# Performance work log

Hardware: AMD Instinct MI355X
Metric: run time of the kernel (lower is better)

The kernel has to match this reference:

```python
import jax, jax.numpy as jnp
import numpy as np

WS = 8          # window_size
NH = 8          # num_heads
IQKV = 128      # inner_qk_v_dim
IQKC = 32       # inner_qk_c_dim
IVV = 64        # inner_v_v_dim
EPS = 1e-6
B, HH, WW, DV, DC = 2, 224, 224, 256, 64


def _rmsnorm(x, g):
    return x * jax.lax.rsqrt(jnp.mean(x * x, axis=-1, keepdims=True) + EPS) * g


def _window(x):
    # (b, h, w, d) -> (b, Wh, Ww, ws*ws, d)
    b, h, w, d = x.shape
    x = x.reshape(b, h // WS, WS, w // WS, WS, d).transpose(0, 1, 3, 2, 4, 5)
    return x.reshape(b, h // WS, w // WS, WS * WS, d)


def _unwindow(x, h, w):
    # (b, N, ws*ws, d) -> (b, h, w, d)
    b, _, _, d = x.shape
    x = x.reshape(b, h // WS, w // WS, WS, WS, d).transpose(0, 1, 3, 2, 4, 5)
    return x.reshape(b, h, w, d)


def _source_qkv(V, C, Wqk_v, bqk_v, g_v, Wqk_c, bqk_c, g_c, Wv):
    Vw, Cw = _window(V), _window(C)          # (b, Wh, Ww, n, d)
    b, Wh, Ww, n, _ = Vw.shape
    N = Wh * Ww
    Vavg, Cavg = Vw.mean(-2), Cw.mean(-2)
    qk_v = _rmsnorm(Vavg @ Wqk_v + bqk_v, g_v)   # (b, Wh, Ww, 2*IQKV)
    qk_c = _rmsnorm(Cavg @ Wqk_c + bqk_c, g_c)   # (b, Wh, Ww, 2*IQKC)
    # 'b Wh Ww (H e) -> b H (Wh Ww) e' then chunk2 along e
    qk_v = qk_v.reshape(b, N, NH, -1).transpose(0, 2, 1, 3)
    qk_c = qk_c.reshape(b, N, NH, -1).transpose(0, 2, 1, 3)
    ev, ec = qk_v.shape[-1] // 2, qk_c.shape[-1] // 2
    qv, kv = qk_v[..., :ev], qk_v[..., ev:]
    qc, kc = qk_c[..., :ec], qk_c[..., ec:]
    # value projection: 'b Wh Ww n (e H) -> b H (Wh Ww) (n e)'
    e = IVV // NH
    Vv = (Vw @ Wv).reshape(b, N, n, e, NH).transpose(0, 4, 1, 2, 3).reshape(b, NH, N, n * e)
    return qv, kv, qc, kc, Vv, (Wh, Ww)


def _forward(values0, coords0, values1, coords1,
             Wqk_v, bqk_v, g_v, Wqk_c, bqk_c, g_c, Wv, Wback):
    parts = [_source_qkv(V, C, Wqk_v, bqk_v, g_v, Wqk_c, bqk_c, g_c, Wv)
             for V, C in ((values0, coords0), (values1, coords1))]
    qv = jnp.concatenate([p[0] for p in parts], axis=2)
    kv = jnp.concatenate([p[1] for p in parts], axis=2)
    qc = jnp.concatenate([p[2] for p in parts], axis=2)
    kc = jnp.concatenate([p[3] for p in parts], axis=2)
    Vv = jnp.concatenate([p[4] for p in parts], axis=2)
    scores = (jnp.einsum('bhqe,bhke->bhqk', qv, kv) / jnp.sqrt(jnp.float32(IQKV))
              + jnp.einsum('bhqe,bhke->bhqk', qc, kc) / jnp.sqrt(jnp.float32(IQKC)))
    A = jax.nn.softmax(scores, axis=-1)            # (b, H, N, N)
    rw = jnp.einsum('bhqk,bhkf->bhqf', A, Vv)      # (b, H, N, n*e)
    b, _, N, _ = rw.shape
    n, e = WS * WS, IVV // NH
    # 'b H N (n e) -> b N n (e H)'
    rw = rw.reshape(b, NH, N, n, e).transpose(0, 2, 3, 4, 1).reshape(b, N, n, e * NH)
    rw = rw @ Wback                                # (b, N, n, Dv)
    outs, off = [], 0
    for (V, _), p in zip(((values0, coords0), (values1, coords1)), parts):
        Wh, Ww = p[5]
        Ns = Wh * Ww
        outs.append(_unwindow(rw[:, off:off + Ns], Wh * WS, Ww * WS))
        off += Ns
    return tuple(outs)


def setup_inputs() -> dict:
    key = jax.random.key(0)
    ks = jax.random.split(key, 8)
    s = 0.02
    return {
        'values0': jax.random.normal(ks[0], (B, HH, WW, DV), jnp.float32),
        'coords0': jax.random.normal(ks[1], (B, HH, WW, DC), jnp.float32),
        'values1': jax.random.normal(ks[2], (B, HH, WW, DV), jnp.float32),
        'coords1': jax.random.normal(ks[3], (B, HH, WW, DC), jnp.float32),
        'Wqk_v': s * jax.random.normal(ks[4], (DV, 2 * IQKV), jnp.float32),
        'bqk_v': jnp.zeros((2 * IQKV,), jnp.float32),
        'g_v': jnp.ones((2 * IQKV,), jnp.float32),
        'Wqk_c': s * jax.random.normal(ks[5], (DC, 2 * IQKC), jnp.float32),
        'bqk_c': jnp.zeros((2 * IQKC,), jnp.float32),
        'g_c': jnp.ones((2 * IQKC,), jnp.float32),
        'Wv': s * jax.random.normal(ks[6], (DV, IVV), jnp.float32),
        'Wback': s * jax.random.normal(ks[7], (IVV, DV), jnp.float32),
    }


def reference(values0, coords0, values1, coords1,
              Wqk_v, bqk_v, g_v, Wqk_c, bqk_c, g_c, Wv, Wback):
    return _forward(values0, coords0, values1, coords1,
                    Wqk_v, bqk_v, g_v, Wqk_c, bqk_c, g_c, Wv, Wback)
```

## Files before the change

### kernel.cpp

```cpp
#include <hip/hip_runtime.h>

#define NSRC 784
#define NTOT 1568
#define NHD 8
#define DVC 256
#define DCC 64
#define D20 20
#define FDIM 512
#define OUT_PER_SRC 25690112

typedef short s16x8 __attribute__((ext_vector_type(8)));
typedef unsigned short u16x8 __attribute__((ext_vector_type(8)));
typedef unsigned short u16x4 __attribute__((ext_vector_type(4)));
typedef float f32x4 __attribute__((ext_vector_type(4)));
typedef float f32x16 __attribute__((ext_vector_type(16)));
typedef unsigned u32x4 __attribute__((ext_vector_type(4)));

__device__ __forceinline__ unsigned short f2bf(float x) {
    unsigned u = __float_as_uint(x);
    unsigned r = (u + 0x7FFFu + ((u >> 16) & 1u)) >> 16;
    return (unsigned short)r;
}

__device__ __forceinline__ unsigned cvt_pk_bf16(float lo, float hi) {
    unsigned r;
    asm volatile("v_cvt_pk_bf16_f32 %0, %1, %2" : "=v"(r) : "v"(lo), "v"(hi));
    return r;
}

__device__ __forceinline__ void split_bf(float x, unsigned short& hi, unsigned short& lo) {
    unsigned short h = f2bf(x);
    float hf = __uint_as_float(((unsigned)h) << 16);
    hi = h;
    lo = f2bf(x - hf);
}

__global__ __launch_bounds__(256) void kz_zero(unsigned short* __restrict__ p) {
    size_t i = (size_t)blockIdx.x * 256 + threadIdx.x;
    u16x8 z = (u16x8)0;
    *(u16x8*)&p[i * 8] = z;
}

__global__ __launch_bounds__(256) void k0c_wvpack(
    const float* __restrict__ Wv, unsigned short* __restrict__ Wvp) {
    int idx = blockIdx.x * 256 + threadIdx.x;
    int j = idx & 7, lane = (idx >> 3) & 63, hl = (idx >> 9) & 1;
    int c = (idx >> 10) & 7, mi = idx >> 13;
    int e = mi * 16 + (lane & 15);
    int dd = c * 32 + (lane >> 4) * 8 + j;
    unsigned short h, l;
    split_bf(Wv[dd * DCC + e], h, l);
    Wvp[idx] = hl ? l : h;
}

__global__ __launch_bounds__(256) void k0b_wback(
    const float* __restrict__ Wb, unsigned short* __restrict__ Wp) {
    int idx = blockIdx.x * 256 + threadIdx.x;
    int jj = idx & 7, lane = (idx >> 3) & 63, hl = (idx >> 9) & 1;
    int kc = (idx >> 10) & 1, mt = idx >> 11;
    int c = mt * 16 + (lane & 15);
    int j = kc * 32 + (lane >> 4) * 8 + jj;
    unsigned short h, l;
    split_bf(Wb[j * 256 + c], h, l);
    Wp[idx] = hl ? l : h;
}

__global__ __launch_bounds__(256) void k1c_avg(
    const float* __restrict__ c0, const float* __restrict__ c1,
    float* __restrict__ Cavg) {
    int wi = blockIdx.x * 4 + (threadIdx.x >> 6);
    int d = threadIdx.x & 63;
    int b = wi / NTOT, N = wi % NTOT;
    int src = N / NSRC, nloc = N % NSRC;
    int wh = nloc / 28, ww = nloc % 28;
    const float* __restrict__ C = src ? c1 : c0;
    int pbase = (b * 224 + wh * 8) * 224 + ww * 8;
    float s = 0.f;
#pragma unroll 8
    for (int p = 0; p < 64; ++p)
        s += C[(size_t)(pbase + (p >> 3) * 224 + (p & 7)) * DCC + d];
    Cavg[(size_t)wi * DCC + d] = s * 0.015625f;
}

__global__ __launch_bounds__(256) void k2_qk(
    const float* __restrict__ Vavg, const float* __restrict__ Cavg,
    const float* __restrict__ Wqkv, const float* __restrict__ bqkv, const float* __restrict__ gv,
    const float* __restrict__ Wqkc, const float* __restrict__ bqkc, const float* __restrict__ gc,
    unsigned short* __restrict__ Qp, unsigned short* __restrict__ Kp) {
    __shared__ float xv[DVC];
    __shared__ float xc[DCC];
    __shared__ float wred[4];
    int blk = blockIdx.x;
    int b = blk / NTOT, N = blk % NTOT;
    int t = threadIdx.x;
    int tile = N >> 5, l31 = N & 31;
    xv[t] = Vavg[(size_t)blk * DVC + t];
    if (t < DCC) xc[t] = Cavg[(size_t)blk * DCC + t];
    __syncthreads();
    float yv = bqkv[t];
#pragma unroll 4
    for (int d = 0; d < DVC; ++d) yv += xv[d] * Wqkv[d * 256 + t];
    float ss = yv * yv;
#pragma unroll
    for (int off = 32; off; off >>= 1) ss += __shfl_xor(ss, off, 64);
    if ((t & 63) == 0) wred[t >> 6] = ss;
    __syncthreads();
    float tot = wred[0] + wred[1] + wred[2] + wred[3];
    float rv = rsqrtf(tot * (1.f / 256.f) + 1e-6f);
    float yn = yv * rv * gv[t];
    int h = t >> 5, c = t & 31;
    int bh = b * NHD + h;
    {
        int isq = (c < 16);
        int d = isq ? c : c - 16;
        float val = isq ? yn * 0.088388347648318447f : yn;
        unsigned short h16, l16;
        split_bf(val, h16, l16);
        int hh = d >> 3, j = d & 7;
        size_t base = ((size_t)(bh * 49 + tile) * 4) * 512 + (size_t)(hh * 32 + l31) * 8 + j;
        unsigned short* dst = isq ? Qp : Kp;
        dst[base] = h16;
        dst[base + 1024] = l16;
    }
    if (t < DCC) {
        float yc = bqkc[t];
#pragma unroll 4
        for (int d = 0; d < DCC; ++d) yc += xc[d] * Wqkc[d * 64 + t];
        float sc = yc * yc;
#pragma unroll
        for (int off = 32; off; off >>= 1) sc += __shfl_xor(sc, off, 64);
        float rc = rsqrtf(sc * (1.f / 64.f) + 1e-6f);
        float ycn = yc * rc * gc[t];
        int h2 = t >> 3, c2 = t & 7;
        int bh2 = b * NHD + h2;
        int isq = (c2 < 4);
        int dd = isq ? c2 : c2 - 4;
        float val = isq ? ycn * 0.17677669529663687f : ycn;
        unsigned short h16, l16;
        split_bf(val, h16, l16);
        size_t base = ((size_t)(bh2 * 49 + tile) * 4 + 1) * 512 + (size_t)l31 * 8 + dd;
        unsigned short* dst = isq ? Qp : Kp;
        dst[base] = h16;
        dst[base + 1024] = l16;
    }
}

__global__ __launch_bounds__(256) void k3_vv(
    const float* __restrict__ v0, const float* __restrict__ v1,
    const unsigned short* __restrict__ Wvp,
    unsigned short* __restrict__ Vvb, float* __restrict__ Vavg) {
    __shared__ unsigned short eb[64 * 66];
    __shared__ float avgw[1024];
    int blk = blockIdx.x;
    int b = blk / NTOT, N = blk % NTOT;
    int src = N / NSRC, nloc = N % NSRC;
    int wh = nloc / 28, ww = nloc % 28;
    const float* __restrict__ V = src ? v1 : v0;
    int t = threadIdx.x;
    int w = t >> 6, lane = t & 63;
    int lm = lane & 15, lk = lane >> 4;
    int px = w * 16 + lm;
    int pbase = (b * 224 + wh * 8) * 224 + ww * 8;
    const float* __restrict__ xrow =
        V + (size_t)(pbase + (px >> 3) * 224 + (px & 7)) * DVC + lk * 8;

    f32x4 acc[4];
#pragma unroll
    for (int mi = 0; mi < 4; ++mi) acc[mi] = (f32x4)0.f;

#pragma unroll
    for (int c = 0; c < 8; ++c) {
        float4 x0 = *(const float4*)&xrow[c * 32];
        float4 x1 = *(const float4*)&xrow[c * 32 + 4];
        float xv8[8] = {x0.x, x0.y, x0.z, x0.w, x1.x, x1.y, x1.z, x1.w};
        u16x8 bhu, blu;
#pragma unroll
        for (int j = 0; j < 8; ++j) {
            unsigned short hq, lq;
            split_bf(xv8[j], hq, lq);
            bhu[j] = hq; blu[j] = lq;
        }
        s16x8 xhi = __builtin_bit_cast(s16x8, bhu);
        s16x8 xlo = __builtin_bit_cast(s16x8, blu);
        float sv[8] = {xv8[0], xv8[1], xv8[2], xv8[3], xv8[4], xv8[5], xv8[6], xv8[7]};
#pragma unroll
        for (int off = 1; off <= 8; off <<= 1)
#pragma unroll
            for (int j = 0; j < 8; ++j) sv[j] += __shfl_xor(sv[j], off, 64);
        if (lm == 0) {
#pragma unroll
            for (int j = 0; j < 8; ++j)
                avgw[w * 256 + c * 32 + lk * 8 + j] = sv[j];
        }
#pragma unroll
        for (int mi = 0; mi < 4; ++mi) {
            const unsigned short* Wf = Wvp + (size_t)((mi * 8 + c) * 2) * 512 + lane * 8;
            s16x8 Ah = *(const s16x8*)&Wf[0];
            s16x8 Al = *(const s16x8*)&Wf[512];
            acc[mi] = __builtin_amdgcn_mfma_f32_16x16x32_bf16(Ah, xlo, acc[mi], 0, 0, 0);
            acc[mi] = __builtin_amdgcn_mfma_f32_16x16x32_bf16(Al, xhi, acc[mi], 0, 0, 0);
            acc[mi] = __builtin_amdgcn_mfma_f32_16x16x32_bf16(Ah, xhi, acc[mi], 0, 0, 0);
        }
    }
#pragma unroll
    for (int mi = 0; mi < 4; ++mi) {
#pragma unroll
        for (int r = 0; r < 4; ++r) {
            int e = mi * 16 + lk * 4 + r;
            eb[px * 66 + e] = f2bf(acc[mi][r]);
        }
    }
    __syncthreads();
    unsigned short* dst = Vvb + (size_t)blk * 4096;
#pragma unroll
    for (int i = 0; i < 2; ++i) {
        int flat16 = i * 256 + t;
        int f3 = flat16 >> 6;
        int h = (flat16 >> 3) & 7;
        int px8 = (flat16 & 7) * 8;
        u16x8 vv;
#pragma unroll
        for (int u = 0; u < 8; ++u) vv[u] = eb[(px8 + u) * 66 + f3 * 8 + h];
        *(u16x8*)&dst[flat16 * 8] = vv;
    }
    Vavg[(size_t)blk * DVC + t] =
        (avgw[t] + avgw[256 + t] + avgw[512 + t] + avgw[768 + t]) * 0.015625f;
}

__global__ __launch_bounds__(256) void k3b_pack(
    const unsigned short* __restrict__ Vvb, unsigned short* __restrict__ Vp) {
    __shared__ unsigned short tile[32 * 576];
    int kt = blockIdx.x, bh = blockIdx.y;
    int b = bh >> 3, h = bh & 7;
    int t = threadIdx.x;
#pragma unroll
    for (int it = 0; it < 8; ++it) {
        int flat = it * 256 + t;
        int r5 = flat >> 6;
        int c = flat & 63;
        int f3 = c >> 3, px8 = (c & 7) * 8;
        const unsigned short* s =
            Vvb + ((size_t)(b * NTOT + kt * 32 + r5) * 8 + f3) * 512 + h * 64 + px8;
        *(u16x8*)&tile[r5 * 576 + f3 * 72 + px8] = *(const u16x8*)s;
    }
    __syncthreads();
    unsigned short* dst = Vp + ((size_t)bh * 49 + kt) * 16384;
#pragma unroll
    for (int it = 0; it < 8; ++it) {
        int flato = it * 256 + t;
        int lane = flato & 63;
        int kh = (flato >> 6) & 1;
        int sub = (flato >> 7) & 3;
        int w = flato >> 9;
        int l31 = lane & 31, hh = lane >> 5;
        int f = w * 128 + sub * 32 + l31;
        int kbase = kh * 16 + hh * 8;
        u16x8 v;
#pragma unroll
        for (int j = 0; j < 8; ++j)
            v[j] = tile[(kbase + j) * 576 + (f & 7) * 72 + (f >> 3)];
        *(u16x8*)&dst[(size_t)flato * 8] = v;
    }
}

__global__ __launch_bounds__(256) void k4_attn(
    const unsigned short* __restrict__ Qp, const unsigned short* __restrict__ Kp,
    const unsigned short* __restrict__ Vp, float* __restrict__ rw) {
    __shared__ float ebuf[32 * 132];
    int wg = blockIdx.x;
    int qt = wg >> 4, bh = wg & 15;
    int q0 = qt * 32;
    int t = threadIdx.x;
    int w = t >> 6, lane = t & 63;
    int l31 = lane & 31, hh = lane >> 5;

    const unsigned short* __restrict__ Qpb = Qp + ((size_t)(bh * 49 + qt) * 4) * 512 + lane * 8;
    const unsigned short* __restrict__ Kpb = Kp + (size_t)bh * 49 * 2048 + lane * 8;
    const unsigned short* __restrict__ Vpb = Vp + (size_t)bh * 49 * 16384 + lane * 8;

    s16x8 qa0 = *(const s16x8*)&Qpb[0];
    s16x8 qa1 = *(const s16x8*)&Qpb[512];
    s16x8 ql0 = *(const s16x8*)&Qpb[1024];
    s16x8 ql1 = *(const s16x8*)&Qpb[1536];

    s16x8 ka0 = *(const s16x8*)&Kpb[0];
    s16x8 ka1 = *(const s16x8*)&Kpb[512];
    s16x8 kl0 = *(const s16x8*)&Kpb[1024];
    s16x8 kl1 = *(const s16x8*)&Kpb[1536];

    float m = -1e30f, lsum = 0.f;
    f32x16 acc[4];
#pragma unroll
    for (int s = 0; s < 4; ++s) acc[s] = (f32x16)0.f;

    for (int kt = 0; kt < NTOT / 32; ++kt) {
        const unsigned short* Vtile = Vpb + (size_t)kt * 16384 + (w * 8) * 512;
        s16x8 va[8];
#pragma unroll
        for (int fr = 0; fr < 8; ++fr)
            va[fr] = *(const s16x8*)&Vtile[fr * 512];
        int ktn = (kt < 48) ? kt + 1 : 48;
        const unsigned short* Ktn = Kpb + (size_t)ktn * 2048;
        s16x8 kn0 = *(const s16x8*)&Ktn[0];
        s16x8 kn1 = *(const s16x8*)&Ktn[512];
        s16x8 kn2 = *(const s16x8*)&Ktn[1024];
        s16x8 kn3 = *(const s16x8*)&Ktn[1536];

        f32x16 sacc = (f32x16)0.f;
        sacc = __builtin_amdgcn_mfma_f32_32x32x16_bf16(kl0, qa0, sacc, 0, 0, 0);
        sacc = __builtin_amdgcn_mfma_f32_32x32x16_bf16(ka0, ql0, sacc, 0, 0, 0);
        sacc = __builtin_amdgcn_mfma_f32_32x32x16_bf16(ka0, qa0, sacc, 0, 0, 0);
        sacc = __builtin_amdgcn_mfma_f32_32x32x16_bf16(kl1, qa1, sacc, 0, 0, 0);
        sacc = __builtin_amdgcn_mfma_f32_32x32x16_bf16(ka1, ql1, sacc, 0, 0, 0);
        sacc = __builtin_amdgcn_mfma_f32_32x32x16_bf16(ka1, qa1, sacc, 0, 0, 0);

        float tmax = sacc[0];
#pragma unroll
        for (int r = 1; r < 16; ++r) tmax = fmaxf(tmax, sacc[r]);
        tmax = fmaxf(tmax, __shfl_xor(tmax, 32, 64));
        if (__any(tmax > m + 8.f)) {
            float mn = fmaxf(m, tmax);
            float sc = __expf(m - mn);
#pragma unroll
            for (int s = 0; s < 4; ++s) acc[s] = acc[s] * sc;
            lsum *= sc;
            m = mn;
        }
        unsigned P2[8];
        float tsum = 0.f;
#pragma unroll
        for (int j = 0; j < 8; ++j) {
            float pa = __expf(sacc[2 * j] - m);
            float pb = __expf(sacc[2 * j + 1] - m);
            tsum += pa + pb;
            P2[j] = cvt_pk_bf16(pa, pb);
        }
        lsum += tsum + __shfl_xor(tsum, 32, 64);
        unsigned X2[8];
#pragma unroll
        for (int j = 0; j < 8; ++j) X2[j] = (unsigned)__shfl_xor((int)P2[j], 32, 64);
        u32x4 b0u, b1u;
        if (hh == 0) {
            b0u[0] = P2[0]; b0u[1] = P2[1]; b0u[2] = X2[0]; b0u[3] = X2[1];
            b1u[0] = P2[4]; b1u[1] = P2[5]; b1u[2] = X2[4]; b1u[3] = X2[5];
        } else {
            b0u[0] = X2[2]; b0u[1] = X2[3]; b0u[2] = P2[2]; b0u[3] = P2[3];
            b1u[0] = X2[6]; b1u[1] = X2[7]; b1u[2] = P2[6]; b1u[3] = P2[7];
        }
        s16x8 pb0 = __builtin_bit_cast(s16x8, b0u);
        s16x8 pb1 = __builtin_bit_cast(s16x8, b1u);

#pragma unroll
        for (int sub = 0; sub < 4; ++sub) {
            acc[sub] = __builtin_amdgcn_mfma_f32_32x32x16_bf16(va[2 * sub],     pb0, acc[sub], 0, 0, 0);
            acc[sub] = __builtin_amdgcn_mfma_f32_32x32x16_bf16(va[2 * sub + 1], pb1, acc[sub], 0, 0, 0);
        }
        ka0 = kn0; ka1 = kn1; kl0 = kn2; kl1 = kn3;
    }

    float inv = 1.f / lsum;
    float* rwg = rw + ((size_t)bh * NTOT + q0) * FDIM;
#pragma unroll
    for (int c = 0; c < 4; ++c) {
        __syncthreads();
        if (w == c) {
#pragma unroll
            for (int sub = 0; sub < 4; ++sub) {
#pragma unroll
                for (int r = 0; r < 16; ++r) {
                    int fl = sub * 32 + (r & 3) + 8 * (r >> 2) + 4 * hh;
                    ebuf[l31 * 132 + fl] = acc[sub][r] * inv;
                }
            }
        }
        __syncthreads();
        int qr = t >> 3, cb = (t & 7) * 16;
#pragma unroll
        for (int j = 0; j < 4; ++j) {
            *(float4*)&rwg[(size_t)qr * FDIM + c * 128 + cb + j * 4] =
                *(const float4*)&ebuf[qr * 132 + cb + j * 4];
        }
    }
}

__global__ __launch_bounds__(256) void k5_back(
    const float* __restrict__ rw, const unsigned short* __restrict__ Wp,
    float* __restrict__ out) {
    __shared__ unsigned short SB[2 * 64 * 72];
    unsigned short* BhL = SB;
    unsigned short* BlL = SB + 64 * 72;
    int blk = blockIdx.x;
    int b = blk / NTOT, N = blk % NTOT;
    int src = N / NSRC, nloc = N % NSRC;
    int wh = nloc / 28, ww = nloc % 28;
    int t = threadIdx.x;
    int w = t >> 6, lane = t & 63;
    int lm = lane & 15, lk = lane >> 4;
    int pbase = (b * 224 + wh * 8) * 224 + ww * 8;

#pragma unroll
    for (int i = 0; i < 4; ++i) {
        int flat4 = i * 256 + t;
        int h = flat4 >> 7;
        int f0 = (flat4 & 127) * 4;
        float4 v = *(const float4*)&rw[((size_t)(b * NHD + h) * NTOT + N) * FDIM + f0];
        int n = f0 >> 3;
        int ebase = f0 & 7;
        float vv[4] = {v.x, v.y, v.z, v.w};
#pragma unroll
        for (int u = 0; u < 4; ++u) {
            int j8 = ebase + u;
            unsigned short h16, l16;
            split_bf(vv[u], h16, l16);
            int col = ((j8 ^ (n & 7)) << 3) | h;
            BhL[n * 72 + col] = h16;
            BlL[n * 72 + col] = l16;
        }
    }
    __syncthreads();

    f32x4 acc[4][4];
#pragma unroll
    for (int mi = 0; mi < 4; ++mi)
#pragma unroll
        for (int nt = 0; nt < 4; ++nt) acc[mi][nt] = (f32x4)0.f;

    const unsigned short* Wpw = Wp + (size_t)(w * 4) * 2048 + lane * 8;
#pragma unroll
    for (int kc = 0; kc < 2; ++kc) {
        s16x8 Ah[4], Al[4], Bh4[4], Bl4[4];
#pragma unroll
        for (int mi = 0; mi < 4; ++mi) {
            int base = mi * 2048 + kc * 1024;
            Ah[mi] = *(const s16x8*)&Wpw[base];
            Al[mi] = *(const s16x8*)&Wpw[base + 512];
        }
#pragma unroll
        for (int nt = 0; nt < 4; ++nt) {
            int n = nt * 16 + lm;
            int addr = n * 72 + (((kc * 4 + lk) ^ (n & 7)) << 3);
            Bh4[nt] = *(const s16x8*)&BhL[addr];
            Bl4[nt] = *(const s16x8*)&BlL[addr];
        }
#pragma unroll
        for (int mi = 0; mi < 4; ++mi)
#pragma unroll
            for (int nt = 0; nt < 4; ++nt) {
                acc[mi][nt] = __builtin_amdgcn_mfma_f32_16x16x32_bf16(Ah[mi], Bl4[nt], acc[mi][nt], 0, 0, 0);
                acc[mi][nt] = __builtin_amdgcn_mfma_f32_16x16x32_bf16(Al[mi], Bh4[nt], acc[mi][nt], 0, 0, 0);
                acc[mi][nt] = __builtin_amdgcn_mfma_f32_16x16x32_bf16(Ah[mi], Bh4[nt], acc[mi][nt], 0, 0, 0);
            }
    }

    float* eb = (float*)SB;
    float* outp = out + (size_t)src * OUT_PER_SRC;
#pragma unroll
    for (int ch = 0; ch < 4; ++ch) {
        __syncthreads();
        if (w == ch) {
#pragma unroll
            for (int mi = 0; mi < 4; ++mi)
#pragma unroll
                for (int nt = 0; nt < 4; ++nt)
#pragma unroll
                    for (int r = 0; r < 4; ++r) {
                        int n = nt * 16 + lm;
                        int cl = mi * 16 + lk * 4 + r;
                        eb[n * 68 + cl] = acc[mi][nt][r];
                    }
        }
        __syncthreads();
#pragma unroll
        for (int i = 0; i < 4; ++i) {
            int fl4 = i * 256 + t;
            int n = fl4 >> 4, c4 = (fl4 & 15) * 4;
            int opix = pbase + (n >> 3) * 224 + (n & 7);
            *(float4*)&outp[(size_t)opix * DVC + ch * 64 + c4] =
                *(const float4*)&eb[n * 68 + c4];
        }
    }
}

extern "C" void kernel_launch(void* const* d_in, const int* in_sizes, int n_in,
                              void* d_out, int out_size, void* d_ws, size_t ws_size,
                              hipStream_t stream) {
    const float* v0   = (const float*)d_in[0];
    const float* c0   = (const float*)d_in[1];
    const float* v1   = (const float*)d_in[2];
    const float* c1   = (const float*)d_in[3];
    const float* Wqkv = (const float*)d_in[4];
    const float* bqkv = (const float*)d_in[5];
    const float* gv   = (const float*)d_in[6];
    const float* Wqkc = (const float*)d_in[7];
    const float* bqkc = (const float*)d_in[8];
    const float* gc   = (const float*)d_in[9];
    const float* Wv   = (const float*)d_in[10];
    const float* Wbk  = (const float*)d_in[11];

    float* ws = (float*)d_ws;
    float* rw   = ws;
    float* Vavg = ws;
    float* Cavg = ws + 802816;
    unsigned short* Qp   = (unsigned short*)(ws + 12845056);
    unsigned short* Kp   = (unsigned short*)(ws + 13647872);
    unsigned short* Wvp  = (unsigned short*)(ws + 14450688);
    unsigned short* Vvb  = (unsigned short*)(ws + 14467072);
    unsigned short* Vp   = (unsigned short*)(ws + 20889600);
    unsigned short* Wp   = (unsigned short*)(ws + 27312128);

    float* outp = (float*)d_out;

    kz_zero   <<<1568, 256, 0, stream>>>(Qp);
    k0c_wvpack<<<256, 256, 0, stream>>>(Wv, Wvp);
    k0b_wback <<<256, 256, 0, stream>>>(Wbk, Wp);
    k3_vv     <<<2 * NTOT, 256, 0, stream>>>(v0, v1, Wvp, Vvb, Vavg);
    k1c_avg   <<<784, 256, 0, stream>>>(c0, c1, Cavg);
    k2_qk     <<<2 * NTOT, 256, 0, stream>>>(Vavg, Cavg, Wqkv, bqkv, gv, Wqkc, bqkc, gc, Qp, Kp);
    k3b_pack  <<<dim3(49, 16), 256, 0, stream>>>(Vvb, Vp);
    k4_attn   <<<784, 256, 0, stream>>>(Qp, Kp, Vp, rw);
    k5_back   <<<2 * NTOT, 256, 0, stream>>>(rw, Wp, outp);
}
```

Baseline: 335.6 us.

## Use exp2 softmax with folded log2e, permlane32 swap, drop K prefetch

Folds log2(e) into the query scaling so the attention softmax can use exp2f instead of __expf, and raises the lazy-rescale threshold to match the base-2 scores. Replaces eight cross-half shuffles plus a branchy select with four v_permlane32_swap instructions to build the P operand. Removes the one-tile-ahead K register prefetch so K loads happen at the top of each iteration, and adds an occupancy hint of 3 blocks to cut register pressure. The risk is exposing K load latency on every iteration, and a threshold shift that could loosen numerical bounds.

```diff
diff --git a/kernel.cpp b/kernel.cpp
--- a/kernel.cpp
+++ b/kernel.cpp
@@ -16,6 +16,8 @@
 typedef float f32x16 __attribute__((ext_vector_type(16)));
 typedef unsigned u32x4 __attribute__((ext_vector_type(4)));
 
+#define LOG2E 1.4426950408889634f
+
 __device__ __forceinline__ unsigned short f2bf(float x) {
     unsigned u = __float_as_uint(x);
     unsigned r = (u + 0x7FFFu + ((u >> 16) & 1u)) >> 16;
@@ -33,6 +35,10 @@
     float hf = __uint_as_float(((unsigned)h) << 16);
     hi = h;
     lo = f2bf(x - hf);
+}
+
+__device__ __forceinline__ void permlane32_swap(unsigned& a, unsigned& b) {
+    asm volatile("v_permlane32_swap_b32 %0, %1" : "+v"(a), "+v"(b));
 }
 
 __global__ __launch_bounds__(256) void kz_zero(unsigned short* __restrict__ p) {
@@ -113,7 +119,7 @@
     {
         int isq = (c < 16);
         int d = isq ? c : c - 16;
-        float val = isq ? yn * 0.088388347648318447f : yn;
+        float val = isq ? yn * (0.088388347648318447f * LOG2E) : yn;
         unsigned short h16, l16;
         split_bf(val, h16, l16);
         int hh = d >> 3, j = d & 7;
@@ -135,7 +141,7 @@
         int bh2 = b * NHD + h2;
         int isq = (c2 < 4);
         int dd = isq ? c2 : c2 - 4;
-        float val = isq ? ycn * 0.17677669529663687f : ycn;
+        float val = isq ? ycn * (0.17677669529663687f * LOG2E) : ycn;
         unsigned short h16, l16;
         split_bf(val, h16, l16);
         size_t base = ((size_t)(bh2 * 49 + tile) * 4 + 1) * 512 + (size_t)l31 * 8 + dd;
@@ -263,7 +269,7 @@
     }
 }
 
-__global__ __launch_bounds__(256) void k4_attn(
+__global__ __launch_bounds__(256, 3) void k4_attn(
     const unsigned short* __restrict__ Qp, const unsigned short* __restrict__ Kp,
     const unsigned short* __restrict__ Vp, float* __restrict__ rw) {
     __shared__ float ebuf[32 * 132];
@@ -283,28 +289,22 @@
     s16x8 ql0 = *(const s16x8*)&Qpb[1024];
     s16x8 ql1 = *(const s16x8*)&Qpb[1536];
 
-    s16x8 ka0 = *(const s16x8*)&Kpb[0];
-    s16x8 ka1 = *(const s16x8*)&Kpb[512];
-    s16x8 kl0 = *(const s16x8*)&Kpb[1024];
-    s16x8 kl1 = *(const s16x8*)&Kpb[1536];
-
     float m = -1e30f, lsum = 0.f;
     f32x16 acc[4];
 #pragma unroll
     for (int s = 0; s < 4; ++s) acc[s] = (f32x16)0.f;
 
     for (int kt = 0; kt < NTOT / 32; ++kt) {
+        const unsigned short* Ktp = Kpb + (size_t)kt * 2048;
+        s16x8 ka0 = *(const s16x8*)&Ktp[0];
+        s16x8 ka1 = *(const s16x8*)&Ktp[512];
+        s16x8 kl0 = *(const s16x8*)&Ktp[1024];
+        s16x8 kl1 = *(const s16x8*)&Ktp[1536];
         const unsigned short* Vtile = Vpb + (size_t)kt * 16384 + (w * 8) * 512;
         s16x8 va[8];
 #pragma unroll
         for (int fr = 0; fr < 8; ++fr)
             va[fr] = *(const s16x8*)&Vtile[fr * 512];
-        int ktn = (kt < 48) ? kt + 1 : 48;
-        const unsigned short* Ktn = Kpb + (size_t)ktn * 2048;
-        s16x8 kn0 = *(const s16x8*)&Ktn[0];
-        s16x8 kn1 = *(const s16x8*)&Ktn[512];
-        s16x8 kn2 = *(const s16x8*)&Ktn[1024];
-        s16x8 kn3 = *(const s16x8*)&Ktn[1536];
 
         f32x16 sacc = (f32x16)0.f;
         sacc = __builtin_amdgcn_mfma_f32_32x32x16_bf16(kl0, qa0, sacc, 0, 0, 0);
@@ -314,13 +314,18 @@
         sacc = __builtin_amdgcn_mfma_f32_32x32x16_bf16(ka1, ql1, sacc, 0, 0, 0);
         sacc = __builtin_amdgcn_mfma_f32_32x32x16_bf16(ka1, qa1, sacc, 0, 0, 0);
 
-        float tmax = sacc[0];
-#pragma unroll
-        for (int r = 1; r < 16; ++r) tmax = fmaxf(tmax, sacc[r]);
+        float t0 = fmaxf(fmaxf(sacc[0], sacc[1]), sacc[2]);
+        float t1 = fmaxf(fmaxf(sacc[3], sacc[4]), sacc[5]);
+        float t2 = fmaxf(fmaxf(sacc[6], sacc[7]), sacc[8]);
+        float t3 = fmaxf(fmaxf(sacc[9], sacc[10]), sacc[11]);
+        float t4 = fmaxf(fmaxf(sacc[12], sacc[13]), sacc[14]);
+        float u0 = fmaxf(fmaxf(t0, t1), t2);
+        float u1 = fmaxf(t3, t4);
+        float tmax = fmaxf(fmaxf(u0, u1), sacc[15]);
         tmax = fmaxf(tmax, __shfl_xor(tmax, 32, 64));
-        if (__any(tmax > m + 8.f)) {
+        if (__any(tmax > m + 11.5f)) {
             float mn = fmaxf(m, tmax);
-            float sc = __expf(m - mn);
+            float sc = exp2f(m - mn);
 #pragma unroll
             for (int s = 0; s < 4; ++s) acc[s] = acc[s] * sc;
             lsum *= sc;
@@ -330,23 +335,19 @@
         float tsum = 0.f;
 #pragma unroll
         for (int j = 0; j < 8; ++j) {
-            float pa = __expf(sacc[2 * j] - m);
-            float pb = __expf(sacc[2 * j + 1] - m);
+            float pa = exp2f(sacc[2 * j] - m);
+            float pb = exp2f(sacc[2 * j + 1] - m);
             tsum += pa + pb;
             P2[j] = cvt_pk_bf16(pa, pb);
         }
         lsum += tsum + __shfl_xor(tsum, 32, 64);
-        unsigned X2[8];
-#pragma unroll
-        for (int j = 0; j < 8; ++j) X2[j] = (unsigned)__shfl_xor((int)P2[j], 32, 64);
+        permlane32_swap(P2[0], P2[2]);
+        permlane32_swap(P2[1], P2[3]);
+        permlane32_swap(P2[4], P2[6]);
+        permlane32_swap(P2[5], P2[7]);
         u32x4 b0u, b1u;
-        if (hh == 0) {
-            b0u[0] = P2[0]; b0u[1] = P2[1]; b0u[2] = X2[0]; b0u[3] = X2[1];
-            b1u[0] = P2[4]; b1u[1] = P2[5]; b1u[2] = X2[4]; b1u[3] = X2[5];
-        } else {
-            b0u[0] = X2[2]; b0u[1] = X2[3]; b0u[2] = P2[2]; b0u[3] = P2[3];
-            b1u[0] = X2[6]; b1u[1] = X2[7]; b1u[2] = P2[6]; b1u[3] = P2[7];
-        }
+        b0u[0] = P2[0]; b0u[1] = P2[1]; b0u[2] = P2[2]; b0u[3] = P2[3];
+        b1u[0] = P2[4]; b1u[1] = P2[5]; b1u[2] = P2[6]; b1u[3] = P2[7];
         s16x8 pb0 = __builtin_bit_cast(s16x8, b0u);
         s16x8 pb1 = __builtin_bit_cast(s16x8, b1u);
 
@@ -355,7 +356,6 @@
             acc[sub] = __builtin_amdgcn_mfma_f32_32x32x16_bf16(va[2 * sub],     pb0, acc[sub], 0, 0, 0);
             acc[sub] = __builtin_amdgcn_mfma_f32_32x32x16_bf16(va[2 * sub + 1], pb1, acc[sub], 0, 0, 0);
         }
-        ka0 = kn0; ka1 = kn1; kl0 = kn2; kl1 = kn3;
     }
 
     float inv = 1.f / lsum;
```

New measurement: 354.0 us. 1.05x slower.
